# Kernel tuning notes

Hardware: AMD Instinct MI355X
Metric: run time of the kernel (lower is better)

The kernel has to match this reference:

```python
import jax, jax.numpy as jnp
import numpy as np

IOU_THRESHOLD = 0.5

def cxcywh_to_xyxy(b):
    cx, cy, w, h = jnp.split(b, 4, axis=-1)
    return jnp.concatenate([cx - 0.5 * w, cy - 0.5 * h, cx + 0.5 * w, cy + 0.5 * h], axis=-1)

def batched_giou(p_xyxy, t_xyxy):
    # p_xyxy: [B, N, 4], t_xyxy: [B, T, 4] -> giou: [B, N, T]
    p = p_xyxy[:, :, None, :]  # [B, N, 1, 4]
    t = t_xyxy[:, None, :, :]  # [B, 1, T, 4]
    area_p = (p_xyxy[..., 2] - p_xyxy[..., 0]) * (p_xyxy[..., 3] - p_xyxy[..., 1])  # [B, N]
    area_t = (t_xyxy[..., 2] - t_xyxy[..., 0]) * (t_xyxy[..., 3] - t_xyxy[..., 1])  # [B, T]
    lt = jnp.maximum(p[..., :2], t[..., :2])
    rb = jnp.minimum(p[..., 2:], t[..., 2:])
    wh = jnp.clip(rb - lt, 0.0)
    inter = wh[..., 0] * wh[..., 1]  # [B, N, T]
    union = area_p[:, :, None] + area_t[:, None, :] - inter
    iou = inter / union
    # enclosing box
    lt_e = jnp.minimum(p[..., :2], t[..., :2])
    rb_e = jnp.maximum(p[..., 2:], t[..., 2:])
    wh_e = jnp.clip(rb_e - lt_e, 0.0)
    area_e = wh_e[..., 0] * wh_e[..., 1]
    return iou - (area_e - union) / area_e

def setup_inputs() -> dict:
    key = jax.random.key(0)
    k1, k2 = jax.random.split(key)
    B, N, T = 128, 900, 300
    pred_boxes = jax.random.uniform(k1, (B, N, 4), dtype=jnp.float32)
    target_boxes = jax.random.uniform(k2, (B, T, 4), dtype=jnp.float32)
    target_mask = jnp.ones((B, T), dtype=bool)
    return {"pred_boxes": pred_boxes, "target_boxes": target_boxes, "target_mask": target_mask}

def reference(pred_boxes, target_boxes, target_mask):
    # pred_boxes: [B, N, 4] cxcywh; target_boxes: [B, T, 4] cxcywh (padded)
    p_xyxy = cxcywh_to_xyxy(pred_boxes)
    t_xyxy = cxcywh_to_xyxy(target_boxes)
    giou = batched_giou(p_xyxy, t_xyxy)  # [B, N, T]
    max_iou = jnp.max(giou, axis=1)      # [B, T] best GIoU per target
    pred_idx = jnp.argmax(giou, axis=1)  # [B, T] matched query per target
    valid = target_mask & (max_iou >= IOU_THRESHOLD)  # [B, T] match kept
    return pred_idx, valid, max_iou
```

## Files before the change

kernel.cpp:

```cpp
#include <hip/hip_runtime.h>


#define BB 128
#define NN 900
#define TT 300
#define TCHUNK 64
#define TBLOCKS 5
#define NSPLIT 9
#define NPB 100
#define NPW 25
#define MARGIN 2e-5f

__device__ __forceinline__ float giou_exact(float4 pb, float4 tb) {
#pragma clang fp contract(off)
    float px0 = pb.x - 0.5f * pb.z, py0 = pb.y - 0.5f * pb.w;
    float px1 = pb.x + 0.5f * pb.z, py1 = pb.y + 0.5f * pb.w;
    float tx0 = tb.x - 0.5f * tb.z, ty0 = tb.y - 0.5f * tb.w;
    float tx1 = tb.x + 0.5f * tb.z, ty1 = tb.y + 0.5f * tb.w;
    float pa = (px1 - px0) * (py1 - py0);
    float ta = (tx1 - tx0) * (ty1 - ty0);
    float w  = fmaxf(fminf(px1, tx1) - fmaxf(px0, tx0), 0.f);
    float h  = fmaxf(fminf(py1, ty1) - fmaxf(py0, ty0), 0.f);
    float inter = w * h;
    float uni   = pa + ta - inter;
    float iou   = inter / uni;
    float ew = fmaxf(fmaxf(px1, tx1) - fminf(px0, tx0), 0.f);
    float eh = fmaxf(fmaxf(py1, ty1) - fminf(py0, ty0), 0.f);
    float ea = ew * eh;
    return iou - (ea - uni) / ea;
}

__global__ __launch_bounds__(256) void matcher_scan_kernel(
    const float* __restrict__ pred,
    const float* __restrict__ tgt,
    float* __restrict__ pbest,
    float* __restrict__ psec,
    int*   __restrict__ pidx)
{
    __shared__ float4 sp[NPB];
    __shared__ float  spa[NPB];
    __shared__ float  rbv[256], rsv[256];
    __shared__ int    riv[256];

    const int ns  = blockIdx.x % NSPLIT;
    const int tc  = (blockIdx.x / NSPLIT) % TBLOCKS;
    const int b   = blockIdx.x / (NSPLIT * TBLOCKS);
    const int tid = threadIdx.x;
    const int tl  = tid & 63;
    const int ng  = tid >> 6;
    const int t   = tc * TCHUNK + tl;

    if (tid < NPB) {
        const float4 pb = ((const float4*)pred)[b * NN + ns * NPB + tid];
        float4 q;
        q.x = pb.x - 0.5f * pb.z;
        q.y = pb.y - 0.5f * pb.w;
        q.z = pb.x + 0.5f * pb.z;
        q.w = pb.y + 0.5f * pb.w;
        sp[tid]  = q;
        spa[tid] = (q.z - q.x) * (q.w - q.y);
    }
    __syncthreads();

    float tx0 = 0.f, ty0 = 0.f, tx1 = 0.f, ty1 = 0.f, ta = 0.f;
    if (t < TT) {
        const float4 tb = ((const float4*)tgt)[b * TT + t];
        tx0 = tb.x - 0.5f * tb.z;
        ty0 = tb.y - 0.5f * tb.w;
        tx1 = tb.x + 0.5f * tb.z;
        ty1 = tb.y + 0.5f * tb.w;
        ta  = (tx1 - tx0) * (ty1 - ty0);
    }

    float best = -INFINITY, second = -INFINITY;
    int   bidx = 0;
    const int k0 = ng * NPW;
    #pragma unroll 5
    for (int k = 0; k < NPW; ++k) {
        const float4 p = sp[k0 + k];
        const float pa = spa[k0 + k];

        const float w   = fmaxf(fminf(p.z, tx1) - fmaxf(p.x, tx0), 0.f);
        const float h   = fmaxf(fminf(p.w, ty1) - fmaxf(p.y, ty0), 0.f);
        const float inter = w * h;
        const float uni   = pa + ta - inter;

        const float ew = fmaxf(p.z, tx1) - fminf(p.x, tx0);
        const float eh = fmaxf(p.w, ty1) - fminf(p.y, ty0);
        const float ea = ew * eh;

        const float num = fmaf(inter, ea, uni * (uni - ea));
        const float g   = num * __builtin_amdgcn_rcpf(uni * ea);

        second = __builtin_amdgcn_fmed3f(g, best, second);
        if (g > best) { bidx = k0 + k; }
        best = fmaxf(best, g);
    }

    rbv[tid] = best; rsv[tid] = second; riv[tid] = bidx;
    __syncthreads();

    if (ng == 0 && t < TT) {
        for (int s = 1; s < 4; ++s) {
            const float ob = rbv[s * 64 + tl];
            const float os = rsv[s * 64 + tl];
            const int   oi = riv[s * 64 + tl];
            second = fmaxf(fminf(best, ob), fmaxf(second, os));
            if (ob > best) { best = ob; bidx = oi; }
        }
        const int bt = b * TT + t;
        pbest[ns * BB * TT + bt] = best;
        psec [ns * BB * TT + bt] = second;
        pidx [ns * BB * TT + bt] = ns * NPB + bidx;
    }
}

__global__ __launch_bounds__(256) void matcher_finish_kernel(
    const float* __restrict__ pbest,
    const float* __restrict__ psec,
    const int*   __restrict__ pidx,
    const float* __restrict__ pred,
    const float* __restrict__ tgt,
    const unsigned char* __restrict__ mask,
    float* __restrict__ out)
{
    __shared__ int sflag[256];
    __shared__ int scount;

    const int tid = threadIdx.x;
    const int bt  = blockIdx.x * 256 + tid;
    if (tid == 0) scount = 0;
    __syncthreads();

    float best = -INFINITY, second = -INFINITY;
    int   bidx = 0;
    for (int s = 0; s < NSPLIT; ++s) {
        const float ob = pbest[s * BB * TT + bt];
        const float os = psec [s * BB * TT + bt];
        const int   oi = pidx [s * BB * TT + bt];
        second = fmaxf(fminf(best, ob), fmaxf(second, os));
        if (ob > best) { best = ob; bidx = oi; }
    }

    if (best - second > MARGIN) {
        const int b = bt / TT;
        const float4 pb = ((const float4*)pred)[b * NN + bidx];
        const float4 tb = ((const float4*)tgt)[bt];
        const float g = giou_exact(pb, tb);
        const bool valid = (mask[bt] != 0) && (g >= 0.5f);
        out[bt]               = (float)bidx;
        out[BB * TT + bt]     = valid ? 1.f : 0.f;
        out[2 * BB * TT + bt] = g;
    } else {
        const int pos = atomicAdd(&scount, 1);
        sflag[pos] = tid;
    }
    __syncthreads();

    const int cnt  = scount;
    const int lane = tid & 63;
    const int ng   = tid >> 6;
    for (int f = ng; f < cnt; f += 4) {
        const int fbt = blockIdx.x * 256 + sflag[f];
        const int b   = fbt / TT;
        const float4 tb = ((const float4*)tgt)[fbt];

        float bestx = -INFINITY;
        int   bix   = NN;
        for (int n = lane; n < NN; n += 64) {
            const float4 pb = ((const float4*)pred)[b * NN + n];
            const float g = giou_exact(pb, tb);
            if (g > bestx) { bestx = g; bix = n; }
        }
        for (int off = 32; off >= 1; off >>= 1) {
            const float ob = __shfl_xor(bestx, off);
            const int   oi = __shfl_xor(bix, off);
            if (ob > bestx || (ob == bestx && oi < bix)) { bestx = ob; bix = oi; }
        }
        if (lane == 0) {
            const bool valid = (mask[fbt] != 0) && (bestx >= 0.5f);
            out[fbt]               = (float)bix;
            out[BB * TT + fbt]     = valid ? 1.f : 0.f;
            out[2 * BB * TT + fbt] = bestx;
        }
    }
}

extern "C" void kernel_launch(void* const* d_in, const int* in_sizes, int n_in,
                              void* d_out, int out_size, void* d_ws, size_t ws_size,
                              hipStream_t stream) {
    const float* pred = (const float*)d_in[0];
    const float* tgt  = (const float*)d_in[1];
    const unsigned char* mask = (const unsigned char*)d_in[2];
    float* out = (float*)d_out;

    const size_t seg = (size_t)NSPLIT * BB * TT * 4;
    char* ws = (char*)d_ws;
    float* pbest = (float*)ws;
    float* psec  = (float*)(ws + seg);
    int*   pidx  = (int*)  (ws + 2 * seg);

    matcher_scan_kernel<<<dim3(BB * TBLOCKS * NSPLIT), dim3(256), 0, stream>>>(
        pred, tgt, pbest, psec, pidx);
    matcher_finish_kernel<<<dim3(BB * TT / 256), dim3(256), 0, stream>>>(
        pbest, psec, pidx, pred, tgt, mask, out);
}
```

Baseline: 95.58 us.

## Register-block five targets per lane to cut block count and LDS reloads

The scan kernel now assigns each block all 300 targets of one batch and prediction chunk, with each lane holding 5 targets in registers (60 active lanes per wave). Each prediction loaded from LDS is reused across 5 targets, and the grid shrinks by a factor of five. The cross-wave reduction moves to a larger shared buffer sized for all targets. In exchange, 4 of 64 lanes sit idle, register pressure rises, and there are fewer blocks to fill the GPU (1152).

```diff
diff --git a/kernel.cpp b/kernel.cpp
--- a/kernel.cpp
+++ b/kernel.cpp
@@ -4,11 +4,11 @@
 #define BB 128
 #define NN 900
 #define TT 300
-#define TCHUNK 64
-#define TBLOCKS 5
 #define NSPLIT 9
 #define NPB 100
 #define NPW 25
+#define TPL 5
+#define ALANES 60
 #define MARGIN 2e-5f
 
 __device__ __forceinline__ float giou_exact(float4 pb, float4 tb) {
@@ -30,7 +30,7 @@
     return iou - (ea - uni) / ea;
 }
 
-__global__ __launch_bounds__(256) void matcher_scan_kernel(
+__global__ __launch_bounds__(256, 6) void matcher_scan_kernel(
     const float* __restrict__ pred,
     const float* __restrict__ tgt,
     float* __restrict__ pbest,
@@ -39,16 +39,14 @@
 {
     __shared__ float4 sp[NPB];
     __shared__ float  spa[NPB];
-    __shared__ float  rbv[256], rsv[256];
-    __shared__ int    riv[256];
+    __shared__ float  sbv[4 * TT], ssv[4 * TT];
+    __shared__ int    siv[4 * TT];
 
     const int ns  = blockIdx.x % NSPLIT;
-    const int tc  = (blockIdx.x / NSPLIT) % TBLOCKS;
-    const int b   = blockIdx.x / (NSPLIT * TBLOCKS);
+    const int b   = blockIdx.x / NSPLIT;
     const int tid = threadIdx.x;
-    const int tl  = tid & 63;
+    const int l   = tid & 63;
     const int ng  = tid >> 6;
-    const int t   = tc * TCHUNK + tl;
 
     if (tid < NPB) {
         const float4 pb = ((const float4*)pred)[b * NN + ns * NPB + tid];
@@ -60,58 +58,76 @@
         sp[tid]  = q;
         spa[tid] = (q.z - q.x) * (q.w - q.y);
     }
-    __syncthreads();
-
-    float tx0 = 0.f, ty0 = 0.f, tx1 = 0.f, ty1 = 0.f, ta = 0.f;
-    if (t < TT) {
-        const float4 tb = ((const float4*)tgt)[b * TT + t];
-        tx0 = tb.x - 0.5f * tb.z;
-        ty0 = tb.y - 0.5f * tb.w;
-        tx1 = tb.x + 0.5f * tb.z;
-        ty1 = tb.y + 0.5f * tb.w;
-        ta  = (tx1 - tx0) * (ty1 - ty0);
-    }
-
-    float best = -INFINITY, second = -INFINITY;
-    int   bidx = 0;
+
+    float tx0[TPL], ty0[TPL], tx1[TPL], ty1[TPL], ta[TPL];
+    #pragma unroll
+    for (int j = 0; j < TPL; ++j) {
+        tx0[j] = ty0[j] = tx1[j] = ty1[j] = ta[j] = 0.f;
+        if (l < ALANES) {
+            const float4 tb = ((const float4*)tgt)[b * TT + j * ALANES + l];
+            tx0[j] = tb.x - 0.5f * tb.z;
+            ty0[j] = tb.y - 0.5f * tb.w;
+            tx1[j] = tb.x + 0.5f * tb.z;
+            ty1[j] = tb.y + 0.5f * tb.w;
+            ta[j]  = (tx1[j] - tx0[j]) * (ty1[j] - ty0[j]);
+        }
+    }
+    __syncthreads();
+
+    float best[TPL], sec[TPL];
+    int   bl[TPL];
+    #pragma unroll
+    for (int j = 0; j < TPL; ++j) { best[j] = -INFINITY; sec[j] = -INFINITY; bl[j] = 0; }
+
     const int k0 = ng * NPW;
-    #pragma unroll 5
     for (int k = 0; k < NPW; ++k) {
         const float4 p = sp[k0 + k];
         const float pa = spa[k0 + k];
-
-        const float w   = fmaxf(fminf(p.z, tx1) - fmaxf(p.x, tx0), 0.f);
-        const float h   = fmaxf(fminf(p.w, ty1) - fmaxf(p.y, ty0), 0.f);
-        const float inter = w * h;
-        const float uni   = pa + ta - inter;
-
-        const float ew = fmaxf(p.z, tx1) - fminf(p.x, tx0);
-        const float eh = fmaxf(p.w, ty1) - fminf(p.y, ty0);
-        const float ea = ew * eh;
-
-        const float num = fmaf(inter, ea, uni * (uni - ea));
-        const float g   = num * __builtin_amdgcn_rcpf(uni * ea);
-
-        second = __builtin_amdgcn_fmed3f(g, best, second);
-        if (g > best) { bidx = k0 + k; }
-        best = fmaxf(best, g);
-    }
-
-    rbv[tid] = best; rsv[tid] = second; riv[tid] = bidx;
-    __syncthreads();
-
-    if (ng == 0 && t < TT) {
-        for (int s = 1; s < 4; ++s) {
-            const float ob = rbv[s * 64 + tl];
-            const float os = rsv[s * 64 + tl];
-            const int   oi = riv[s * 64 + tl];
-            second = fmaxf(fminf(best, ob), fmaxf(second, os));
-            if (ob > best) { best = ob; bidx = oi; }
-        }
-        const int bt = b * TT + t;
-        pbest[ns * BB * TT + bt] = best;
-        psec [ns * BB * TT + bt] = second;
-        pidx [ns * BB * TT + bt] = ns * NPB + bidx;
+        #pragma unroll
+        for (int j = 0; j < TPL; ++j) {
+            const float w   = fmaxf(fminf(p.z, tx1[j]) - fmaxf(p.x, tx0[j]), 0.f);
+            const float h   = fmaxf(fminf(p.w, ty1[j]) - fmaxf(p.y, ty0[j]), 0.f);
+            const float inter = w * h;
+            const float uni   = pa + ta[j] - inter;
+            const float ew  = fmaxf(p.z, tx1[j]) - fminf(p.x, tx0[j]);
+            const float eh  = fmaxf(p.w, ty1[j]) - fminf(p.y, ty0[j]);
+            const float ea  = ew * eh;
+            const float den = uni * ea;
+            const float num = fmaf(inter, ea, fmaf(uni, uni, -den));
+            const float g   = num * __builtin_amdgcn_rcpf(den);
+
+            sec[j] = __builtin_amdgcn_fmed3f(g, best[j], sec[j]);
+            if (g > best[j]) bl[j] = k;
+            best[j] = fmaxf(best[j], g);
+        }
+    }
+
+    if (l < ALANES) {
+        #pragma unroll
+        for (int j = 0; j < TPL; ++j) {
+            const int u = j * ALANES + l;
+            sbv[ng * TT + u] = best[j];
+            ssv[ng * TT + u] = sec[j];
+            siv[ng * TT + u] = k0 + bl[j];
+        }
+    }
+    __syncthreads();
+
+    for (int u = tid; u < TT; u += 256) {
+        float bb = -INFINITY, ss = -INFINITY;
+        int   bi = 0;
+        #pragma unroll
+        for (int s = 0; s < 4; ++s) {
+            const float ob = sbv[s * TT + u];
+            const float os = ssv[s * TT + u];
+            const int   oi = siv[s * TT + u];
+            ss = fmaxf(fminf(bb, ob), fmaxf(ss, os));
+            if (ob > bb) { bb = ob; bi = oi; }
+        }
+        const int bt = b * TT + u;
+        pbest[ns * BB * TT + bt] = bb;
+        psec [ns * BB * TT + bt] = ss;
+        pidx [ns * BB * TT + bt] = ns * NPB + bi;
     }
 }
 
@@ -134,6 +150,7 @@
 
     float best = -INFINITY, second = -INFINITY;
     int   bidx = 0;
+    #pragma unroll
     for (int s = 0; s < NSPLIT; ++s) {
         const float ob = pbest[s * BB * TT + bt];
         const float os = psec [s * BB * TT + bt];
@@ -200,7 +217,7 @@
     float* psec  = (float*)(ws + seg);
     int*   pidx  = (int*)  (ws + 2 * seg);
 
-    matcher_scan_kernel<<<dim3(BB * TBLOCKS * NSPLIT), dim3(256), 0, stream>>>(
+    matcher_scan_kernel<<<dim3(BB * NSPLIT), dim3(256), 0, stream>>>(
         pred, tgt, pbest, psec, pidx);
     matcher_finish_kernel<<<dim3(BB * TT / 256), dim3(256), 0, stream>>>(
         pbest, psec, pidx, pred, tgt, mask, out);
```

Measured after the change: 98.54 us. +3.1%, slower.
